# Performance work log

Measured on AMD Instinct MI355X. Metric: run time of the kernel, lower is better.

Reference implementation:

```python
import jax, jax.numpy as jnp
import numpy as np

NUM_FIELDS = 40
# upper-triangular (i<j) field pair indices, computed once at trace time
_I_IDX, _J_IDX = np.triu_indices(NUM_FIELDS, k=1)  # each length 780


def setup_inputs() -> dict:
    key = jax.random.key(0)
    k1, k2 = jax.random.split(key)
    batch, num_fields, embed_dim = 8192, NUM_FIELDS, 32
    num_interactions = num_fields * (num_fields - 1) // 2  # 780
    embeddings = jax.random.normal(k1, (batch, num_fields, embed_dim), dtype=jnp.float32)
    W = jax.random.normal(k2, (num_interactions, embed_dim, embed_dim), dtype=jnp.float32)
    return {"embeddings": embeddings, "W": W}


def reference(embeddings, W):
    # embeddings: (b, f, e); W: (k, e, e) with k = f*(f-1)/2
    vi = embeddings[:, _I_IDX, :]  # (b, k, e)
    vj = embeddings[:, _J_IDX, :]  # (b, k, e)
    # per-pair bilinear form, reduced over embed dims -> (b, k)
    return jnp.einsum('bke,kef,bkf->bk', vi, W, vj)
```

## Files before the change

### kernel.cpp

```cpp
#include <hip/hip_runtime.h>
#include <cstdint>
#include <cstddef>

typedef __attribute__((ext_vector_type(8))) short short8;
typedef __attribute__((ext_vector_type(4))) unsigned short ushort4_t;
typedef __attribute__((ext_vector_type(16))) float f32x16;

#define NF 40
#define NK 780
#define BT 64
#define THREADS 1024

__device__ __forceinline__ unsigned short f2bf(float f) {
    unsigned int u = __float_as_uint(f);
    u = (u + 0x7fffu + ((u >> 16) & 1u)) >> 16;
    return (unsigned short)u;
}
__device__ __forceinline__ float bf2f(unsigned short x) {
    return __uint_as_float(((unsigned int)x) << 16);
}

__global__ __launch_bounds__(128) void wprep_kernel(const float* __restrict__ W,
                                                    unsigned short* __restrict__ wfrag) {
    const int k = blockIdx.x, t = threadIdx.x;
    const int half = t >> 6, l = t & 63;
    const int e = l & 31;
    const int f0 = 16 * half + 8 * (l >> 5);
    const float* src = W + (size_t)k * 1024 + e * 32 + f0;
    const float4 x0 = *(const float4*)src;
    const float4 x1 = *(const float4*)(src + 4);
    short8 v;
    v[0] = (short)f2bf(x0.x); v[1] = (short)f2bf(x0.y);
    v[2] = (short)f2bf(x0.z); v[3] = (short)f2bf(x0.w);
    v[4] = (short)f2bf(x1.x); v[5] = (short)f2bf(x1.y);
    v[6] = (short)f2bf(x1.z); v[7] = (short)f2bf(x1.w);
    *(short8*)(wfrag + (size_t)k * 1024 + half * 512 + l * 8) = v;
}

__device__ __forceinline__ void ld_w4(short8& r0, short8& r1, short8& r2, short8& r3,
                                      const char* addr) {
    asm volatile("global_load_dwordx4 %0, %4, off\n\t"
                 "global_load_dwordx4 %1, %4, off offset:1024\n\t"
                 "global_load_dwordx4 %2, %4, off offset:2048\n\t"
                 "global_load_dwordx4 %3, %4, off offset:3072"
                 : "=&v"(r0), "=&v"(r1), "=&v"(r2), "=&v"(r3)
                 : "v"(addr));
}
#define WAITP() do { asm volatile("s_waitcnt vmcnt(4)" ::: "memory"); \
                     __builtin_amdgcn_sched_barrier(0); } while (0)

#define LOADW2(R0, R1, R2, R3, KB)                                                      \
    {                                                                                   \
        const int kbc = (KB) > 778 ? 778 : (KB);                                        \
        ld_w4(R0, R1, R2, R3, wbase + ((size_t)kbc << 11));                             \
    }


#define RELOAD_VI()                                                                     \
    {                                                                                   \
        const int i7 = ii & 7;                                                          \
        const char* ibase = embT + (ii << 12) + eoff;                                   \
        const ushort4_t a0_ = *(const ushort4_t*)(ibase + (((b32      ) ^ i7) << 4));   \
        const ushort4_t a1_ = *(const ushort4_t*)(ibase + (((b32 +  64) ^ i7) << 4));   \
        const ushort4_t a2_ = *(const ushort4_t*)(ibase + (((b32 + 128) ^ i7) << 4));   \
        const ushort4_t a3_ = *(const ushort4_t*)(ibase + (((b32 + 192) ^ i7) << 4));   \
        const ushort4_t b0_ = *(const ushort4_t*)(ibase + (((b32 +  32) ^ i7) << 4));   \
        const ushort4_t b1_ = *(const ushort4_t*)(ibase + (((b32 +  96) ^ i7) << 4));   \
        const ushort4_t b2_ = *(const ushort4_t*)(ibase + (((b32 + 160) ^ i7) << 4));   \
        const ushort4_t b3_ = *(const ushort4_t*)(ibase + (((b32 + 224) ^ i7) << 4));   \
        uA0 = bf2f(a0_[0]); uA1 = bf2f(a0_[1]); uA2  = bf2f(a0_[2]); uA3  = bf2f(a0_[3]); \
        uA4 = bf2f(a1_[0]); uA5 = bf2f(a1_[1]); uA6  = bf2f(a1_[2]); uA7  = bf2f(a1_[3]); \
        uA8 = bf2f(a2_[0]); uA9 = bf2f(a2_[1]); uA10 = bf2f(a2_[2]); uA11 = bf2f(a2_[3]); \
        uA12 = bf2f(a3_[0]); uA13 = bf2f(a3_[1]); uA14 = bf2f(a3_[2]); uA15 = bf2f(a3_[3]); \
        uB0 = bf2f(b0_[0]); uB1 = bf2f(b0_[1]); uB2  = bf2f(b0_[2]); uB3  = bf2f(b0_[3]); \
        uB4 = bf2f(b1_[0]); uB5 = bf2f(b1_[1]); uB6  = bf2f(b1_[2]); uB7  = bf2f(b1_[3]); \
        uB8 = bf2f(b2_[0]); uB9 = bf2f(b2_[1]); uB10 = bf2f(b2_[2]); uB11 = bf2f(b2_[3]); \
        uB12 = bf2f(b3_[0]); uB13 = bf2f(b3_[1]); uB14 = bf2f(b3_[2]); uB15 = bf2f(b3_[3]); \
    }

#define DOT16(T, V0, V1, V2, V3, V4, V5, V6, V7, V8, V9, V10, V11, V12, V13, V14, V15, P) \
    {                                                                                   \
        float c0 = T[0] * V0;                                                           \
        c0 = __builtin_fmaf(T[1], V1, c0);                                              \
        c0 = __builtin_fmaf(T[2], V2, c0);                                              \
        c0 = __builtin_fmaf(T[3], V3, c0);                                              \
        float c1 = T[4] * V4;                                                           \
        c1 = __builtin_fmaf(T[5], V5, c1);                                              \
        c1 = __builtin_fmaf(T[6], V6, c1);                                              \
        c1 = __builtin_fmaf(T[7], V7, c1);                                              \
        float c2 = T[8] * V8;                                                           \
        c2 = __builtin_fmaf(T[9], V9, c2);                                              \
        c2 = __builtin_fmaf(T[10], V10, c2);                                            \
        c2 = __builtin_fmaf(T[11], V11, c2);                                            \
        float c3 = T[12] * V12;                                                         \
        c3 = __builtin_fmaf(T[13], V13, c3);                                            \
        c3 = __builtin_fmaf(T[14], V14, c3);                                            \
        c3 = __builtin_fmaf(T[15], V15, c3);                                            \
        P = (c0 + c1) + (c2 + c3);                                                      \
        P += __shfl_xor(P, 32);                                                         \
    }

#define KSTEP(A0, A1, OA, OB)                                                           \
    {                                                                                   \
        const int j7 = jj & 7;                                                          \
        const char* jbase = embT + (jj << 12);                                          \
        const short8 vjA0 = *(const short8*)(jbase + (((b32 +       fh0) ^ j7) << 4));  \
        const short8 vjA1 = *(const short8*)(jbase + (((b32 + 128 + fh0) ^ j7) << 4));  \
        const short8 vjB0 = *(const short8*)(jbase + (((b32 + 32  + fh0) ^ j7) << 4));  \
        const short8 vjB1 = *(const short8*)(jbase + (((b32 + 160 + fh0) ^ j7) << 4));  \
        f32x16 tA = __builtin_amdgcn_mfma_f32_32x32x16_bf16(A0, vjA0, zacc, 0, 0, 0);   \
        tA = __builtin_amdgcn_mfma_f32_32x32x16_bf16(A1, vjA1, tA, 0, 0, 0);            \
        f32x16 tB = __builtin_amdgcn_mfma_f32_32x32x16_bf16(A0, vjB0, zacc, 0, 0, 0);   \
        tB = __builtin_amdgcn_mfma_f32_32x32x16_bf16(A1, vjB1, tB, 0, 0, 0);            \
        DOT16(tA, uA0, uA1, uA2, uA3, uA4, uA5, uA6, uA7,                               \
                  uA8, uA9, uA10, uA11, uA12, uA13, uA14, uA15, OA);                    \
        DOT16(tB, uB0, uB1, uB2, uB3, uB4, uB5, uB6, uB7,                               \
                  uB8, uB9, uB10, uB11, uB12, uB13, uB14, uB15, OB);                    \
        ++jj;                                                                           \
        if (jj == NF) { ++ii; jj = ii + 1; RELOAD_VI(); }                               \
    }

__global__ __launch_bounds__(THREADS, 4) void bil_kernel(const float* __restrict__ emb,
                                                         const unsigned short* __restrict__ wfrag,
                                                         float* __restrict__ out) {
    __shared__ __align__(16) char embT[NF * 4096];

    const int tid = threadIdx.x;
    const int b0 = blockIdx.x * BT;

    for (int u = tid; u < BT * 160; u += THREADS) {
        const int bb = u / 160;
        const int t = u - 160 * bb;
        const int field = t >> 2;
        const int fq = t & 3;
        const float* src = emb + (size_t)(b0 + bb) * (NF * 32) + field * 32 + 8 * fq;
        const float4 x0 = *(const float4*)src;
        const float4 x1 = *(const float4*)(src + 4);
        short8 v;
        v[0] = (short)f2bf(x0.x); v[1] = (short)f2bf(x0.y);
        v[2] = (short)f2bf(x0.z); v[3] = (short)f2bf(x0.w);
        v[4] = (short)f2bf(x1.x); v[5] = (short)f2bf(x1.y);
        v[6] = (short)f2bf(x1.z); v[7] = (short)f2bf(x1.w);
        const int g = (bb + 64 * fq) ^ (field & 7);
        *(short8*)(embT + field * 4096 + g * 16) = v;
    }
    __syncthreads();

    const int ww = tid >> 6;
    const int l = tid & 63;
    const int b32 = l & 31;
    const int h32 = l >> 5;
    const int fh0 = 64 * h32;
    const int eoff = 8 * h32;

    const f32x16 zacc = {};

    const int ks = 4 * ((195 * ww) >> 4);
    const int ke = 4 * ((195 * (ww + 1)) >> 4);

    int ii = 0, jj;
    {
        int kk = ks, len = 39;
        while (kk >= len) { kk -= len; ++ii; --len; }
        jj = ii + 1 + kk;
    }

    float uA0, uA1, uA2, uA3, uA4, uA5, uA6, uA7;
    float uA8, uA9, uA10, uA11, uA12, uA13, uA14, uA15;
    float uB0, uB1, uB2, uB3, uB4, uB5, uB6, uB7;
    float uB8, uB9, uB10, uB11, uB12, uB13, uB14, uB15;
    RELOAD_VI();

    const char* wbase = (const char*)wfrag + l * 16;

    short8 a0, a1, a2, a3;
    short8 c0, c1, c2, c3;
    LOADW2(a0, a1, a2, a3, ks);

    const size_t orowoff = (size_t)(b0 + 32 * h32 + b32) * NK;

    for (int kcur = ks; kcur < ke; kcur += 4) {
        float oA0, oA1, oA2, oA3, oB0, oB1, oB2, oB3;
        LOADW2(c0, c1, c2, c3, kcur + 2);
        WAITP();
        KSTEP(a0, a1, oA0, oB0);
        KSTEP(a2, a3, oA1, oB1);
        LOADW2(a0, a1, a2, a3, kcur + 4);
        WAITP();
        KSTEP(c0, c1, oA2, oB2);
        KSTEP(c2, c3, oA3, oB3);
        float4 s;
        if (h32 == 0) { s.x = oA0; s.y = oA1; s.z = oA2; s.w = oA3; }
        else          { s.x = oB0; s.y = oB1; s.z = oB2; s.w = oB3; }
        *(float4*)(out + orowoff + kcur) = s;
    }
}

extern "C" void kernel_launch(void* const* d_in, const int* in_sizes, int n_in,
                              void* d_out, int out_size, void* d_ws, size_t ws_size,
                              hipStream_t stream) {
    const float* emb = (const float*)d_in[0];
    const float* W   = (const float*)d_in[1];
    float* out = (float*)d_out;
    unsigned short* wfrag = (unsigned short*)d_ws;

    wprep_kernel<<<dim3(NK), dim3(128), 0, stream>>>(W, wfrag);
    bil_kernel<<<dim3(8192 / BT), dim3(THREADS), 0, stream>>>(emb, wfrag, out);
}
```

Measured before the change: 48.17 us.

## Split interaction pairs across two blocks per batch tile and unroll main loop

The grid is doubled so each batch tile of 64 rows is handled by two blocks, each covering half of the 780 field pairs. This raises the block count from 128 to 256 to fill more of the GPU's compute units. The main loop is unrolled to process 8 pairs per iteration with two float4 stores, and tail paths handle leftover pairs. In exchange, each block still stages the full embedding tile into shared memory, so that conversion and load work is done twice per tile.

```diff
diff --git a/kernel.cpp b/kernel.cpp
--- a/kernel.cpp
+++ b/kernel.cpp
@@ -10,6 +10,7 @@
 #define NK 780
 #define BT 64
 #define THREADS 1024
+#define KSPLIT 2
 
 __device__ __forceinline__ unsigned short f2bf(float f) {
     unsigned int u = __float_as_uint(f);
@@ -47,6 +48,8 @@
                  : "v"(addr));
 }
 #define WAITP() do { asm volatile("s_waitcnt vmcnt(4)" ::: "memory"); \
+                     __builtin_amdgcn_sched_barrier(0); } while (0)
+#define WAIT0() do { asm volatile("s_waitcnt vmcnt(0)" ::: "memory"); \
                      __builtin_amdgcn_sched_barrier(0); } while (0)
 
 #define LOADW2(R0, R1, R2, R3, KB)                                                      \
@@ -80,23 +83,23 @@
 
 #define DOT16(T, V0, V1, V2, V3, V4, V5, V6, V7, V8, V9, V10, V11, V12, V13, V14, V15, P) \
     {                                                                                   \
-        float c0 = T[0] * V0;                                                           \
-        c0 = __builtin_fmaf(T[1], V1, c0);                                              \
-        c0 = __builtin_fmaf(T[2], V2, c0);                                              \
-        c0 = __builtin_fmaf(T[3], V3, c0);                                              \
-        float c1 = T[4] * V4;                                                           \
-        c1 = __builtin_fmaf(T[5], V5, c1);                                              \
-        c1 = __builtin_fmaf(T[6], V6, c1);                                              \
-        c1 = __builtin_fmaf(T[7], V7, c1);                                              \
-        float c2 = T[8] * V8;                                                           \
-        c2 = __builtin_fmaf(T[9], V9, c2);                                              \
-        c2 = __builtin_fmaf(T[10], V10, c2);                                            \
-        c2 = __builtin_fmaf(T[11], V11, c2);                                            \
-        float c3 = T[12] * V12;                                                         \
-        c3 = __builtin_fmaf(T[13], V13, c3);                                            \
-        c3 = __builtin_fmaf(T[14], V14, c3);                                            \
-        c3 = __builtin_fmaf(T[15], V15, c3);                                            \
-        P = (c0 + c1) + (c2 + c3);                                                      \
+        float d0 = T[0] * V0;                                                           \
+        d0 = __builtin_fmaf(T[1], V1, d0);                                              \
+        d0 = __builtin_fmaf(T[2], V2, d0);                                              \
+        d0 = __builtin_fmaf(T[3], V3, d0);                                              \
+        float d1 = T[4] * V4;                                                           \
+        d1 = __builtin_fmaf(T[5], V5, d1);                                              \
+        d1 = __builtin_fmaf(T[6], V6, d1);                                              \
+        d1 = __builtin_fmaf(T[7], V7, d1);                                              \
+        float d2 = T[8] * V8;                                                           \
+        d2 = __builtin_fmaf(T[9], V9, d2);                                              \
+        d2 = __builtin_fmaf(T[10], V10, d2);                                            \
+        d2 = __builtin_fmaf(T[11], V11, d2);                                            \
+        float d3 = T[12] * V12;                                                         \
+        d3 = __builtin_fmaf(T[13], V13, d3);                                            \
+        d3 = __builtin_fmaf(T[14], V14, d3);                                            \
+        d3 = __builtin_fmaf(T[15], V15, d3);                                            \
+        P = (d0 + d1) + (d2 + d3);                                                      \
         P += __shfl_xor(P, 32);                                                         \
     }
 
@@ -126,7 +129,9 @@
     __shared__ __align__(16) char embT[NF * 4096];
 
     const int tid = threadIdx.x;
-    const int b0 = blockIdx.x * BT;
+    const int btile = blockIdx.x >> 1;
+    const int khalf = blockIdx.x & 1;
+    const int b0 = btile * BT;
 
     for (int u = tid; u < BT * 160; u += THREADS) {
         const int bb = u / 160;
@@ -155,12 +160,13 @@
 
     const f32x16 zacc = {};
 
-    const int ks = 4 * ((195 * ww) >> 4);
-    const int ke = 4 * ((195 * (ww + 1)) >> 4);
+    const int ppbase = khalf * 195;
+    const int ps = ppbase + 2 * ((195 * ww) >> 5);
+    const int pe = ppbase + ((ww == 15) ? 195 : 2 * ((195 * (ww + 1)) >> 5));
 
     int ii = 0, jj;
     {
-        int kk = ks, len = 39;
+        int kk = 2 * ps, len = 39;
         while (kk >= len) { kk -= len; ++ii; --len; }
         jj = ii + 1 + kk;
     }
@@ -173,26 +179,62 @@
 
     const char* wbase = (const char*)wfrag + l * 16;
 
-    short8 a0, a1, a2, a3;
-    short8 c0, c1, c2, c3;
-    LOADW2(a0, a1, a2, a3, ks);
+    short8 aw0, aw1, aw2, aw3;
+    short8 bw0, bw1, bw2, bw3;
+    LOADW2(aw0, aw1, aw2, aw3, 2 * ps);
 
     const size_t orowoff = (size_t)(b0 + 32 * h32 + b32) * NK;
 
-    for (int kcur = ks; kcur < ke; kcur += 4) {
+    int pp = ps;
+    for (; pp + 4 <= pe; pp += 4) {
+        const int kcur = 2 * pp;
+        float oA0, oA1, oA2, oA3, oA4, oA5, oA6, oA7;
+        float oB0, oB1, oB2, oB3, oB4, oB5, oB6, oB7;
+        LOADW2(bw0, bw1, bw2, bw3, kcur + 2);
+        WAITP();
+        KSTEP(aw0, aw1, oA0, oB0);  KSTEP(aw2, aw3, oA1, oB1);
+        LOADW2(aw0, aw1, aw2, aw3, kcur + 4);
+        WAITP();
+        KSTEP(bw0, bw1, oA2, oB2);  KSTEP(bw2, bw3, oA3, oB3);
+        LOADW2(bw0, bw1, bw2, bw3, kcur + 6);
+        WAITP();
+        KSTEP(aw0, aw1, oA4, oB4);  KSTEP(aw2, aw3, oA5, oB5);
+        LOADW2(aw0, aw1, aw2, aw3, kcur + 8);
+        WAITP();
+        KSTEP(bw0, bw1, oA6, oB6);  KSTEP(bw2, bw3, oA7, oB7);
+        float4 s0, s1;
+        if (h32 == 0) { s0.x = oA0; s0.y = oA1; s0.z = oA2; s0.w = oA3;
+                        s1.x = oA4; s1.y = oA5; s1.z = oA6; s1.w = oA7; }
+        else          { s0.x = oB0; s0.y = oB1; s0.z = oB2; s0.w = oB3;
+                        s1.x = oB4; s1.y = oB5; s1.z = oB6; s1.w = oB7; }
+        float* orow = out + orowoff + kcur;
+        *(float4*)orow = s0;
+        *(float4*)(orow + 4) = s1;
+    }
+    if (pp + 2 <= pe) {
+        const int kcur = 2 * pp;
         float oA0, oA1, oA2, oA3, oB0, oB1, oB2, oB3;
-        LOADW2(c0, c1, c2, c3, kcur + 2);
-        WAITP();
-        KSTEP(a0, a1, oA0, oB0);
-        KSTEP(a2, a3, oA1, oB1);
-        LOADW2(a0, a1, a2, a3, kcur + 4);
-        WAITP();
-        KSTEP(c0, c1, oA2, oB2);
-        KSTEP(c2, c3, oA3, oB3);
-        float4 s;
-        if (h32 == 0) { s.x = oA0; s.y = oA1; s.z = oA2; s.w = oA3; }
-        else          { s.x = oB0; s.y = oB1; s.z = oB2; s.w = oB3; }
-        *(float4*)(out + orowoff + kcur) = s;
+        LOADW2(bw0, bw1, bw2, bw3, kcur + 2);
+        WAITP();
+        KSTEP(aw0, aw1, oA0, oB0);  KSTEP(aw2, aw3, oA1, oB1);
+        LOADW2(aw0, aw1, aw2, aw3, kcur + 4);
+        WAITP();
+        KSTEP(bw0, bw1, oA2, oB2);  KSTEP(bw2, bw3, oA3, oB3);
+        float4 s0;
+        if (h32 == 0) { s0.x = oA0; s0.y = oA1; s0.z = oA2; s0.w = oA3; }
+        else          { s0.x = oB0; s0.y = oB1; s0.z = oB2; s0.w = oB3; }
+        *(float4*)(out + orowoff + kcur) = s0;
+        pp += 2;
+    }
+    if (pp < pe) {
+        const int kcur = 2 * pp;
+        float oA0, oA1, oB0, oB1;
+        WAIT0();
+        KSTEP(aw0, aw1, oA0, oB0);  KSTEP(aw2, aw3, oA1, oB1);
+        float2 s0;
+        if (h32 == 0) { s0.x = oA0; s0.y = oA1; }
+        else          { s0.x = oB0; s0.y = oB1; }
+        *(float2*)(out + orowoff + kcur) = s0;
     }
 }
 
@@ -205,5 +247,5 @@
     unsigned short* wfrag = (unsigned short*)d_ws;
 
     wprep_kernel<<<dim3(NK), dim3(128), 0, stream>>>(W, wfrag);
-    bil_kernel<<<dim3(8192 / BT), dim3(THREADS), 0, stream>>>(emb, wfrag, out);
-}
+    bil_kernel<<<dim3((8192 / BT) * KSPLIT), dim3(THREADS), 0, stream>>>(emb, wfrag, out);
+}
```

Result: slower. 56.91 us (+18.2%).
